# Performance work log

Hardware: AMD Instinct MI355X
Metric: run time of the kernel (lower is better)

The kernel has to match this reference:

```python
import math
import jax, jax.numpy as jnp
import numpy as np

B, D, CTX, HID, NSTEPS = 16384, 16, 256, 192, 10
IN_DIM = D + CTX + 1  # 273
DT = -0.1  # integrate t: 1 -> 0 in 10 fixed RK4 steps


def setup_inputs() -> dict:
    key = jax.random.key(0)
    ks = jax.random.split(key, 9)
    rn = lambda k, shape, sc=1.0: jax.random.normal(k, shape, dtype=jnp.float32) * sc
    return {
        "theta": rn(ks[0], (B, D)),
        "h": rn(ks[1], (B, CTX)),
        "eps": rn(ks[2], (NSTEPS, 4, B, D)),  # fresh Hutchinson noise per RK4 stage
        "W1": rn(ks[3], (IN_DIM, HID), 0.5 / np.sqrt(IN_DIM)),
        "b1": jnp.zeros((HID,), jnp.float32),
        "W2": rn(ks[4], (HID, HID), 0.5 / np.sqrt(HID)),
        "b2": jnp.zeros((HID,), jnp.float32),
        "W3": rn(ks[5], (HID, D), 0.5 / np.sqrt(HID)),
        "b3": jnp.zeros((D,), jnp.float32),
    }


def _mlp(x, W1, b1, W2, b2, W3, b3):
    # CNF_MLP depth=2: Linear->GELU->Linear->GELU->Linear (exact erf GELU, torch default)
    h1 = jax.nn.gelu(x @ W1 + b1, approximate=False)
    h2 = jax.nn.gelu(h1 @ W2 + b2, approximate=False)
    return h2 @ W3 + b3


def reference(theta, h, eps, W1, b1, W2, b2, W3, b3):
    """ConditionalCNF.log_prob: RK4 (torchdiffeq 3/8 variant) from t=1 to t=0
    with Hutchinson trace estimator via JVP (eps^T J eps)."""
    dt = jnp.float32(DT)

    def vf(t, y, e):
        def net(y_):
            tf = jnp.full((y_.shape[0], 1), t, y_.dtype)
            return _mlp(jnp.concatenate([y_, h, tf], axis=1), W1, b1, W2, b2, W3, b3)
        f, Je = jax.jvp(net, (y,), (e,))  # Je = J @ e
        trace = jnp.sum(e * Je, axis=1)   # eps^T J eps == (J^T eps) . eps
        return f, -trace

    def step(carry, xs):
        y, logp = carry
        t, e4 = xs  # e4: (4, B, D)
        f1, l1 = vf(t, y, e4[0])
        f2, l2 = vf(t + dt / 3, y + dt * f1 / 3, e4[1])
        f3, l3 = vf(t + 2 * dt / 3, y + dt * (f2 - f1 / 3), e4[2])
        f4, l4 = vf(t + dt, y + dt * (f1 - f2 + f3), e4[3])
        y2 = y + dt * (f1 + 3 * (f2 + f3) + f4) * 0.125
        lp2 = logp + dt * (l1 + 3 * (l2 + l3) + l4) * 0.125
        return (y2, lp2), None

    ts = jnp.float32(1.0) + dt * jnp.arange(NSTEPS, dtype=jnp.float32)
    logp0 = jnp.zeros((theta.shape[0],), theta.dtype)
    (z0, dlogp), _ = jax.lax.scan(step, (theta, logp0), (ts, eps))
    base = -0.5 * jnp.sum(z0 ** 2, axis=1) - 0.5 * D * math.log(2 * math.pi)
    return base - dlogp
```

## Files before the change

### kernel.cpp

```cpp
#include <hip/hip_runtime.h>
#include <math.h>


#define DTc (-0.1f)

typedef __attribute__((ext_vector_type(8))) short bf16x8;
typedef __attribute__((ext_vector_type(8))) unsigned short u16x8;
typedef __attribute__((ext_vector_type(4))) float f32x4;

#define MFMA16(a, b, c) __builtin_amdgcn_mfma_f32_16x16x32_bf16((a), (b), (c), 0, 0, 0)

__device__ __forceinline__ unsigned short f2bf(float x) {
    union { float f; unsigned int u; } c; c.f = x;
    unsigned int r = c.u + 0x7FFFu + ((c.u >> 16) & 1u);
    return (unsigned short)(r >> 16);
}

__device__ __forceinline__ unsigned int pk2bf(float lo, float hi) {
#if __has_builtin(__builtin_amdgcn_cvt_pk_bf16_f32)
    auto v = __builtin_amdgcn_cvt_pk_bf16_f32(lo, hi);
    return __builtin_bit_cast(unsigned int, v);
#else
    return (unsigned int)f2bf(lo) | ((unsigned int)f2bf(hi) << 16);
#endif
}

__device__ __forceinline__ void gelu_both(float x, float& gv, float& dv) {
    float z  = fabsf(x) * 0.70710678118654752f;
    float e  = __builtin_amdgcn_exp2f(x * x * -0.72134752044448170f);
    float t  = __builtin_amdgcn_rcpf(__builtin_fmaf(0.3275911f, z, 1.0f));
    float p  = t * (0.127414796f + t * (-0.142248368f + t * (0.710706871f +
               t * (-0.726576014f + t * 0.530702715f))));
    float ch = p * e;
    float cdf = (x >= 0.0f) ? (1.0f - ch) : ch;
    gv = x * cdf;
    dv = __builtin_fmaf(0.39894228040143268f * x, e, cdf);
}

__global__ void repack_kernel(const float* __restrict__ W1, const float* __restrict__ W2,
                              const float* __restrict__ W3,
                              unsigned short* __restrict__ w2f, unsigned short* __restrict__ w1yf,
                              unsigned short* __restrict__ w1cf, unsigned short* __restrict__ w3fg) {
    int t = blockIdx.x * 256 + threadIdx.x;
    u16x8 v;
    if (t < 4608) {
        int kb = t / 768, rem = t % 768, nt = rem / 64, lane = rem % 64;
        int n = nt * 16 + (lane & 15), k0 = kb * 32 + (lane >> 4) * 8;
        #pragma unroll
        for (int j = 0; j < 8; ++j) v[j] = f2bf(W2[(k0 + j) * 192 + n]);
        *(u16x8*)(w2f + t * 8) = v;
    } else if (t < 5376) {
        int i2 = t - 4608, nt = i2 / 64, lane = i2 % 64;
        int n = nt * 16 + (lane & 15), k0 = (lane >> 4) * 8;
        #pragma unroll
        for (int j = 0; j < 8; ++j) {
            int k = k0 + j;
            v[j] = (k < 16) ? f2bf(W1[k * 192 + n]) : (unsigned short)0;
        }
        *(u16x8*)(w1yf + i2 * 8) = v;
    } else if (t < 11520) {
        int i3 = t - 5376, kb = i3 / 768, rem = i3 % 768, nt = rem / 64, lane = rem % 64;
        int n = nt * 16 + (lane & 15), k0 = kb * 32 + (lane >> 4) * 8;
        #pragma unroll
        for (int j = 0; j < 8; ++j) v[j] = f2bf(W1[(16 + k0 + j) * 192 + n]);
        *(u16x8*)(w1cf + i3 * 8) = v;
    } else if (t < 11904) {
        int i4 = t - 11520, kb = i4 / 64, lane = i4 % 64;
        int n = lane & 15, k0 = kb * 32 + (lane >> 4) * 8;
        #pragma unroll
        for (int j = 0; j < 8; ++j) v[j] = f2bf(W3[(k0 + j) * 16 + n]);
        *(u16x8*)(w3fg + i4 * 8) = v;
    }
}

__global__ __launch_bounds__(256, 2) void cnf_mfma(
    const float* __restrict__ theta, const float* __restrict__ hctx,
    const float* __restrict__ eps,   const float* __restrict__ W1,
    const float* __restrict__ b1,    const float* __restrict__ b2,
    const float* __restrict__ b3,
    const unsigned short* __restrict__ w2f, const unsigned short* __restrict__ w1yf,
    const unsigned short* __restrict__ w1cf, const unsigned short* __restrict__ w3fg,
    float* __restrict__ out)
{
    __shared__ __align__(16) unsigned short Y[64 * 40];
    __shared__ __align__(16) unsigned short Xa0[64 * 200];
    __shared__ __align__(16) unsigned short Xa1[64 * 200];
    __shared__ __align__(16) float ebf[2][512];
    __shared__ float trx[32];

    const int tid  = threadIdx.x;
    const int wave = tid >> 6, lane = tid & 63;
    const int l15  = lane & 15, quad = lane >> 4;
    const int r0   = blockIdx.x * 32;
    const int ntg0 = wave * 3;

    for (int i = tid; i < 64 * 40; i += 256) Y[i] = 0;

    unsigned short* Hs = Xa0;
    for (int t4 = tid; t4 < 2048; t4 += 256) {
        int r = t4 >> 6, k = (t4 & 63) * 4;
        float4 v = *(const float4*)(hctx + (long)(r0 + r) * 256 + k);
        *(uint2*)(&Hs[r * 264 + k]) = make_uint2(pk2bf(v.x, v.y), pk2bf(v.z, v.w));
    }

    const int  ek = ((wave - 2) * 64 + lane) * 4;
    const int  er = ek >> 4, ed = ek & 15;
    const long epsBase = (long)r0 * 16 + ek;
    float4 epr;
    if (wave >= 2) epr = *(const float4*)(eps + epsBase);

    bf16x8 b1yfr[3], w3fr[6];
    #pragma unroll
    for (int nt = 0; nt < 3; ++nt)
        b1yfr[nt] = *reinterpret_cast<const bf16x8*>(w1yf + ((ntg0 + nt) * 64 + lane) * 8);
    #pragma unroll
    for (int kb = 0; kb < 6; ++kb)
        w3fr[kb] = *reinterpret_cast<const bf16x8*>(w3fg + (kb * 64 + lane) * 8);
    float w1tr[3], b2r[3], b1r[3];
    #pragma unroll
    for (int nt = 0; nt < 3; ++nt) {
        int n = (ntg0 + nt) * 16 + l15;
        w1tr[nt] = W1[272 * 192 + n];
        b2r[nt]  = b2[n];
        b1r[nt]  = b1[n];
    }
    const float b3r = b3[l15];

    float yreg[2][4];
    if (wave == 0) {
        #pragma unroll
        for (int mt = 0; mt < 2; ++mt)
            #pragma unroll
            for (int i = 0; i < 4; ++i)
                yreg[mt][i] = theta[(r0 + mt * 16 + quad * 4 + i) * 16 + l15];
    }

    __syncthreads();

    float cr[2][3][4];
    {
        f32x4 ca[2][3] = {};
        #pragma unroll
        for (int kb = 0; kb < 8; ++kb) {
            bf16x8 af[2];
            #pragma unroll
            for (int mt = 0; mt < 2; ++mt)
                af[mt] = *reinterpret_cast<const bf16x8*>(&Hs[(mt * 16 + l15) * 264 + kb * 32 + quad * 8]);
            #pragma unroll
            for (int nt = 0; nt < 3; ++nt) {
                bf16x8 bf = *reinterpret_cast<const bf16x8*>(w1cf + ((kb * 12 + ntg0 + nt) * 64 + lane) * 8);
                #pragma unroll
                for (int mt = 0; mt < 2; ++mt)
                    ca[mt][nt] = MFMA16(af[mt], bf, ca[mt][nt]);
            }
        }
        #pragma unroll
        for (int mt = 0; mt < 2; ++mt)
            #pragma unroll
            for (int nt = 0; nt < 3; ++nt)
                #pragma unroll
                for (int i = 0; i < 4; ++i)
                    cr[mt][nt][i] = ca[mt][nt][i] + b1r[nt];
    }

    if (wave == 0) {
        #pragma unroll
        for (int mt = 0; mt < 2; ++mt)
            #pragma unroll
            for (int i = 0; i < 4; ++i)
                Y[(mt * 16 + quad * 4 + i) * 40 + l15] = f2bf(yreg[mt][i]);
    }
    if (wave >= 2) {
        *(uint2*)(&Y[(32 + er) * 40 + ed]) = make_uint2(pk2bf(epr.x, epr.y), pk2bf(epr.z, epr.w));
        *(float4*)(&ebf[0][ek]) = epr;
        epr = *(const float4*)(eps + (long)1 * 262144 + epsBase);
    }

    float F1[2][4], F2[2][4], F3[2][4];
    float tracc[2][4] = {{0.f,0.f,0.f,0.f},{0.f,0.f,0.f,0.f}};

    for (int sg = 0; sg < 40; ++sg) {
        const int sub = sg & 3;
        const float ts = 1.0f + DTc * (float)(sg >> 2) + DTc * ((float)sub * (1.0f / 3.0f));

        __syncthreads();

        {
            bf16x8 af[4];
            #pragma unroll
            for (int mt = 0; mt < 4; ++mt)
                af[mt] = *reinterpret_cast<const bf16x8*>(&Y[(mt * 16 + l15) * 40 + quad * 8]);
            f32x4 acc[4][3] = {};
            #pragma unroll
            for (int nt = 0; nt < 3; ++nt)
                #pragma unroll
                for (int mt = 0; mt < 4; ++mt)
                    acc[mt][nt] = MFMA16(af[mt], b1yfr[nt], acc[mt][nt]);
            #pragma unroll
            for (int nt = 0; nt < 3; ++nt) {
                int n = (ntg0 + nt) * 16 + l15;
                #pragma unroll
                for (int mt = 0; mt < 2; ++mt) {
                    float gvv[4], dvv[4];
                    #pragma unroll
                    for (int i = 0; i < 4; ++i) {
                        float a = acc[mt][nt][i] + cr[mt][nt][i] + ts * w1tr[nt];
                        float gv, dv; gelu_both(a, gv, dv);
                        gvv[i] = gv; dvv[i] = dv * acc[mt + 2][nt][i];
                    }
                    unsigned int p0 = pk2bf(gvv[0], gvv[1]), p1 = pk2bf(gvv[2], gvv[3]);
                    unsigned int q0 = pk2bf(dvv[0], dvv[1]), q1 = pk2bf(dvv[2], dvv[3]);
                    int ba = (mt * 16 + quad * 4) * 200 + n;
                    Xa0[ba]          = (unsigned short)p0;
                    Xa0[ba + 200]    = (unsigned short)(p0 >> 16);
                    Xa0[ba + 400]    = (unsigned short)p1;
                    Xa0[ba + 600]    = (unsigned short)(p1 >> 16);
                    Xa0[ba + 6400]   = (unsigned short)q0;
                    Xa0[ba + 6600]   = (unsigned short)(q0 >> 16);
                    Xa0[ba + 6800]   = (unsigned short)q1;
                    Xa0[ba + 7000]   = (unsigned short)(q1 >> 16);
                }
            }
        }
        __syncthreads();

        {
            f32x4 acc2[4][3] = {};
            #pragma unroll
            for (int kb = 0; kb < 6; ++kb) {
                bf16x8 aA[4];
                #pragma unroll
                for (int mt = 0; mt < 4; ++mt)
                    aA[mt] = *reinterpret_cast<const bf16x8*>(&Xa0[(mt * 16 + l15) * 200 + kb * 32 + quad * 8]);
                #pragma unroll
                for (int nt = 0; nt < 3; ++nt) {
                    bf16x8 bf = *reinterpret_cast<const bf16x8*>(w2f + ((kb * 12 + ntg0 + nt) * 64 + lane) * 8);
                    #pragma unroll
                    for (int mt = 0; mt < 4; ++mt)
                        acc2[mt][nt] = MFMA16(aA[mt], bf, acc2[mt][nt]);
                }
            }
            #pragma unroll
            for (int nt = 0; nt < 3; ++nt) {
                int n = (ntg0 + nt) * 16 + l15;
                #pragma unroll
                for (int mt = 0; mt < 2; ++mt) {
                    float gvv[4], dvv[4];
                    #pragma unroll
                    for (int i = 0; i < 4; ++i) {
                        float a = acc2[mt][nt][i] + b2r[nt];
                        float gv, dv; gelu_both(a, gv, dv);
                        gvv[i] = gv; dvv[i] = dv * acc2[mt + 2][nt][i];
                    }
                    unsigned int p0 = pk2bf(gvv[0], gvv[1]), p1 = pk2bf(gvv[2], gvv[3]);
                    unsigned int q0 = pk2bf(dvv[0], dvv[1]), q1 = pk2bf(dvv[2], dvv[3]);
                    int ba = (mt * 16 + quad * 4) * 200 + n;
                    Xa1[ba]          = (unsigned short)p0;
                    Xa1[ba + 200]    = (unsigned short)(p0 >> 16);
                    Xa1[ba + 400]    = (unsigned short)p1;
                    Xa1[ba + 600]    = (unsigned short)(p1 >> 16);
                    Xa1[ba + 6400]   = (unsigned short)q0;
                    Xa1[ba + 6600]   = (unsigned short)(q0 >> 16);
                    Xa1[ba + 6800]   = (unsigned short)q1;
                    Xa1[ba + 7000]   = (unsigned short)(q1 >> 16);
                }
            }
        }
        __syncthreads();

        if (wave < 2) {
            f32x4 acc3[2] = {};
            #pragma unroll
            for (int kb = 0; kb < 6; ++kb)
                #pragma unroll
                for (int mt = 0; mt < 2; ++mt) {
                    bf16x8 af = *reinterpret_cast<const bf16x8*>(
                        &Xa1[(wave * 32 + mt * 16 + l15) * 200 + kb * 32 + quad * 8]);
                    acc3[mt] = MFMA16(af, w3fr[kb], acc3[mt]);
                }

            if (wave == 0) {
                float Fc[2][4];
                #pragma unroll
                for (int mt = 0; mt < 2; ++mt)
                    #pragma unroll
                    for (int i = 0; i < 4; ++i) Fc[mt][i] = acc3[mt][i] + b3r;
                if (sub == 0) {
                    #pragma unroll
                    for (int mt = 0; mt < 2; ++mt)
                        for (int i = 0; i < 4; ++i) F1[mt][i] = Fc[mt][i];
                } else if (sub == 1) {
                    #pragma unroll
                    for (int mt = 0; mt < 2; ++mt)
                        for (int i = 0; i < 4; ++i) F2[mt][i] = Fc[mt][i];
                } else if (sub == 2) {
                    #pragma unroll
                    for (int mt = 0; mt < 2; ++mt)
                        for (int i = 0; i < 4; ++i) F3[mt][i] = Fc[mt][i];
                } else {
                    #pragma unroll
                    for (int mt = 0; mt < 2; ++mt)
                        #pragma unroll
                        for (int i = 0; i < 4; ++i)
                            yreg[mt][i] += DTc * 0.125f *
                                (F1[mt][i] + 3.0f * (F2[mt][i] + F3[mt][i]) + Fc[mt][i]);
                }
                if (sg < 39) {
                    const int sub2 = (sg + 1) & 3;
                    #pragma unroll
                    for (int mt = 0; mt < 2; ++mt)
                        #pragma unroll
                        for (int i = 0; i < 4; ++i) {
                            float ys = yreg[mt][i];
                            if (sub2 == 1)      ys += DTc * (1.0f / 3.0f) * F1[mt][i];
                            else if (sub2 == 2) ys += DTc * (F2[mt][i] - (1.0f / 3.0f) * F1[mt][i]);
                            else if (sub2 == 3) ys += DTc * (F1[mt][i] - F2[mt][i] + F3[mt][i]);
                            Y[(mt * 16 + quad * 4 + i) * 40 + l15] = f2bf(ys);
                        }
                }
            } else {
                const float csub = (sub == 1 || sub == 2) ? 3.0f : 1.0f;
                #pragma unroll
                for (int mt = 0; mt < 2; ++mt)
                    #pragma unroll
                    for (int i = 0; i < 4; ++i) {
                        int r = mt * 16 + quad * 4 + i;
                        float p = ebf[sg & 1][r * 16 + l15] * acc3[mt][i];
                        p += __shfl_xor(p, 1);
                        p += __shfl_xor(p, 2);
                        p += __shfl_xor(p, 4);
                        p += __shfl_xor(p, 8);
                        tracc[mt][i] += csub * p;
                    }
            }
        } else {
            if (sg < 39) {
                *(uint2*)(&Y[(32 + er) * 40 + ed]) = make_uint2(pk2bf(epr.x, epr.y), pk2bf(epr.z, epr.w));
                *(float4*)(&ebf[(sg + 1) & 1][ek]) = epr;
                if (sg < 38)
                    epr = *(const float4*)(eps + (long)(sg + 2) * 262144 + epsBase);
            }
        }
    }

    if (wave == 1 && l15 == 0) {
        #pragma unroll
        for (int mt = 0; mt < 2; ++mt)
            #pragma unroll
            for (int i = 0; i < 4; ++i) trx[mt * 16 + quad * 4 + i] = tracc[mt][i];
    }
    __syncthreads();
    if (wave == 0) {
        #pragma unroll
        for (int mt = 0; mt < 2; ++mt)
            #pragma unroll
            for (int i = 0; i < 4; ++i) {
                float q = yreg[mt][i] * yreg[mt][i];
                q += __shfl_xor(q, 1);
                q += __shfl_xor(q, 2);
                q += __shfl_xor(q, 4);
                q += __shfl_xor(q, 8);
                if (l15 == 0)
                    out[r0 + mt * 16 + quad * 4 + i] =
                        -0.5f * q - 14.7030165313f + DTc * 0.125f * trx[mt * 16 + quad * 4 + i];
            }
    }
}

extern "C" void kernel_launch(void* const* d_in, const int* in_sizes, int n_in,
                              void* d_out, int out_size, void* d_ws, size_t ws_size,
                              hipStream_t stream) {
    const float* theta = (const float*)d_in[0];
    const float* hctx  = (const float*)d_in[1];
    const float* eps   = (const float*)d_in[2];
    const float* W1    = (const float*)d_in[3];
    const float* b1    = (const float*)d_in[4];
    const float* W2    = (const float*)d_in[5];
    const float* b2    = (const float*)d_in[6];
    const float* W3    = (const float*)d_in[7];
    const float* b3    = (const float*)d_in[8];
    float* outp = (float*)d_out;

    unsigned short* w2f  = (unsigned short*)d_ws;
    unsigned short* w1yf = w2f + 36864;
    unsigned short* w1cf = w1yf + 6144;
    unsigned short* w3fg = w1cf + 49152;

    hipLaunchKernelGGL(repack_kernel, dim3(47), dim3(256), 0, stream,
                       W1, W2, W3, w2f, w1yf, w1cf, w3fg);
    hipLaunchKernelGGL(cnf_mfma, dim3(512), dim3(256), 0, stream,
                       theta, hctx, eps, W1, b1, b2, b3, w2f, w1yf, w1cf, w3fg, outp);
}
```

Measured before the change: 400.1 us.

## Compute Hutchinson trace via W3ᵀε projection, drop layer-3 tangent GEMM

The trace eps^T J eps is now computed as a dot product of the layer-2 tangent with W3ᵀε, done by a small MFMA. This removes the second-layer tangent rows from the layer-3 GEMM and from shared memory, and makes Xa1 half as large. The time input is folded into the layer-1 MFMA as an extra K column, and eps is loaded straight into registers with prefetch instead of being staged through LDS by two dedicated waves. The erf polynomial is also cut to a lower-order approximation (3 terms), which trades GELU accuracy for fewer instructions.

```diff
diff --git a/kernel.cpp b/kernel.cpp
--- a/kernel.cpp
+++ b/kernel.cpp
@@ -28,9 +28,8 @@
 __device__ __forceinline__ void gelu_both(float x, float& gv, float& dv) {
     float z  = fabsf(x) * 0.70710678118654752f;
     float e  = __builtin_amdgcn_exp2f(x * x * -0.72134752044448170f);
-    float t  = __builtin_amdgcn_rcpf(__builtin_fmaf(0.3275911f, z, 1.0f));
-    float p  = t * (0.127414796f + t * (-0.142248368f + t * (0.710706871f +
-               t * (-0.726576014f + t * 0.530702715f))));
+    float t  = __builtin_amdgcn_rcpf(__builtin_fmaf(0.47047f, z, 1.0f));
+    float p  = t * (0.1740121f + t * (-0.0479399f + t * 0.3739278f));
     float ch = p * e;
     float cdf = (x >= 0.0f) ? (1.0f - ch) : ch;
     gv = x * cdf;
@@ -40,7 +39,8 @@
 __global__ void repack_kernel(const float* __restrict__ W1, const float* __restrict__ W2,
                               const float* __restrict__ W3,
                               unsigned short* __restrict__ w2f, unsigned short* __restrict__ w1yf,
-                              unsigned short* __restrict__ w1cf, unsigned short* __restrict__ w3fg) {
+                              unsigned short* __restrict__ w1cf, unsigned short* __restrict__ w3fg,
+                              unsigned short* __restrict__ w3tf) {
     int t = blockIdx.x * 256 + threadIdx.x;
     u16x8 v;
     if (t < 4608) {
@@ -55,7 +55,8 @@
         #pragma unroll
         for (int j = 0; j < 8; ++j) {
             int k = k0 + j;
-            v[j] = (k < 16) ? f2bf(W1[k * 192 + n]) : (unsigned short)0;
+            v[j] = (k < 16) ? f2bf(W1[k * 192 + n])
+                 : (k == 16) ? f2bf(W1[272 * 192 + n]) : (unsigned short)0;
         }
         *(u16x8*)(w1yf + i2 * 8) = v;
     } else if (t < 11520) {
@@ -70,31 +71,40 @@
         #pragma unroll
         for (int j = 0; j < 8; ++j) v[j] = f2bf(W3[(k0 + j) * 16 + n]);
         *(u16x8*)(w3fg + i4 * 8) = v;
+    } else if (t < 12672) {
+        int i5 = t - 11904, nt = i5 / 64, lane = i5 % 64;
+        int h = nt * 16 + (lane & 15), quad = lane >> 4;
+        #pragma unroll
+        for (int j = 0; j < 8; ++j) {
+            int d = quad * 8 + j;
+            v[j] = (d < 16) ? f2bf(W3[h * 16 + d]) : (unsigned short)0;
+        }
+        *(u16x8*)(w3tf + i5 * 8) = v;
     }
 }
 
 __global__ __launch_bounds__(256, 2) void cnf_mfma(
     const float* __restrict__ theta, const float* __restrict__ hctx,
-    const float* __restrict__ eps,   const float* __restrict__ W1,
-    const float* __restrict__ b1,    const float* __restrict__ b2,
-    const float* __restrict__ b3,
+    const float* __restrict__ eps,   const float* __restrict__ b1,
+    const float* __restrict__ b2,    const float* __restrict__ b3,
     const unsigned short* __restrict__ w2f, const unsigned short* __restrict__ w1yf,
     const unsigned short* __restrict__ w1cf, const unsigned short* __restrict__ w3fg,
+    const unsigned short* __restrict__ w3tf,
     float* __restrict__ out)
 {
-    __shared__ __align__(16) unsigned short Y[64 * 40];
+    __shared__ __align__(16) unsigned short Ys[32 * 24];
     __shared__ __align__(16) unsigned short Xa0[64 * 200];
-    __shared__ __align__(16) unsigned short Xa1[64 * 200];
-    __shared__ __align__(16) float ebf[2][512];
-    __shared__ float trx[32];
+    __shared__ __align__(16) unsigned short Xa1[32 * 200];
+    __shared__ float trrow[32];
 
     const int tid  = threadIdx.x;
     const int wave = tid >> 6, lane = tid & 63;
     const int l15  = lane & 15, quad = lane >> 4;
     const int r0   = blockIdx.x * 32;
     const int ntg0 = wave * 3;
-
-    for (int i = tid; i < 64 * 40; i += 256) Y[i] = 0;
+    const int mt3  = wave - 2;
+
+    if (tid < 32) trrow[tid] = 0.0f;
 
     unsigned short* Hs = Xa0;
     for (int t4 = tid; t4 < 2048; t4 += 256) {
@@ -103,36 +113,42 @@
         *(uint2*)(&Hs[r * 264 + k]) = make_uint2(pk2bf(v.x, v.y), pk2bf(v.z, v.w));
     }
 
-    const int  ek = ((wave - 2) * 64 + lane) * 4;
-    const int  er = ek >> 4, ed = ek & 15;
-    const long epsBase = (long)r0 * 16 + ek;
-    float4 epr;
-    if (wave >= 2) epr = *(const float4*)(eps + epsBase);
-
     bf16x8 b1yfr[3], w3fr[6];
     #pragma unroll
     for (int nt = 0; nt < 3; ++nt)
         b1yfr[nt] = *reinterpret_cast<const bf16x8*>(w1yf + ((ntg0 + nt) * 64 + lane) * 8);
-    #pragma unroll
-    for (int kb = 0; kb < 6; ++kb)
-        w3fr[kb] = *reinterpret_cast<const bf16x8*>(w3fg + (kb * 64 + lane) * 8);
-    float w1tr[3], b2r[3], b1r[3];
+    if (wave >= 2) {
+        #pragma unroll
+        for (int kb = 0; kb < 6; ++kb)
+            w3fr[kb] = *reinterpret_cast<const bf16x8*>(w3fg + (kb * 64 + lane) * 8);
+    }
+    float b2r[3], b1r[3];
     #pragma unroll
     for (int nt = 0; nt < 3; ++nt) {
         int n = (ntg0 + nt) * 16 + l15;
-        w1tr[nt] = W1[272 * 192 + n];
-        b2r[nt]  = b2[n];
-        b1r[nt]  = b1[n];
+        b2r[nt] = b2[n];
+        b1r[nt] = b1[n];
     }
     const float b3r = b3[l15];
 
-    float yreg[2][4];
-    if (wave == 0) {
-        #pragma unroll
-        for (int mt = 0; mt < 2; ++mt)
-            #pragma unroll
-            for (int i = 0; i < 4; ++i)
-                yreg[mt][i] = theta[(r0 + mt * 16 + quad * 4 + i) * 16 + l15];
+    float yreg[4];
+    if (wave >= 2) {
+        #pragma unroll
+        for (int i = 0; i < 4; ++i)
+            yreg[i] = theta[(r0 + mt3 * 16 + quad * 4 + i) * 16 + l15];
+    }
+
+    bf16x8 e0 = {}, e1 = {};
+    if (quad < 2) {
+        const float* ep = eps + ((long)r0 + l15) * 16 + quad * 8;
+        float4 a0 = *(const float4*)ep,          a1 = *(const float4*)(ep + 4);
+        float4 b0 = *(const float4*)(ep + 256),  b4 = *(const float4*)(ep + 260);
+        union { unsigned int u[4]; bf16x8 v; } c0, c1;
+        c0.u[0] = pk2bf(a0.x, a0.y); c0.u[1] = pk2bf(a0.z, a0.w);
+        c0.u[2] = pk2bf(a1.x, a1.y); c0.u[3] = pk2bf(a1.z, a1.w);
+        c1.u[0] = pk2bf(b0.x, b0.y); c1.u[1] = pk2bf(b0.z, b0.w);
+        c1.u[2] = pk2bf(b4.x, b4.y); c1.u[3] = pk2bf(b4.z, b4.w);
+        e0 = c0.v; e1 = c1.v;
     }
 
     __syncthreads();
@@ -163,207 +179,201 @@
                     cr[mt][nt][i] = ca[mt][nt][i] + b1r[nt];
     }
 
-    if (wave == 0) {
-        #pragma unroll
-        for (int mt = 0; mt < 2; ++mt)
-            #pragma unroll
-            for (int i = 0; i < 4; ++i)
-                Y[(mt * 16 + quad * 4 + i) * 40 + l15] = f2bf(yreg[mt][i]);
-    }
     if (wave >= 2) {
-        *(uint2*)(&Y[(32 + er) * 40 + ed]) = make_uint2(pk2bf(epr.x, epr.y), pk2bf(epr.z, epr.w));
-        *(float4*)(&ebf[0][ek]) = epr;
-        epr = *(const float4*)(eps + (long)1 * 262144 + epsBase);
-    }
-
-    float F1[2][4], F2[2][4], F3[2][4];
+        #pragma unroll
+        for (int i = 0; i < 4; ++i)
+            Ys[(mt3 * 16 + quad * 4 + i) * 24 + l15] = f2bf(yreg[i]);
+    }
+
+    float F1[4], F2[4], F3[4];
     float tracc[2][4] = {{0.f,0.f,0.f,0.f},{0.f,0.f,0.f,0.f}};
 
     for (int sg = 0; sg < 40; ++sg) {
         const int sub = sg & 3;
         const float ts = 1.0f + DTc * (float)(sg >> 2) + DTc * ((float)sub * (1.0f / 3.0f));
+        const short tsb = (short)f2bf(ts);
 
         __syncthreads();
 
+        bf16x8 aY0 = {}, aY1 = {};
+        if (quad < 2) {
+            aY0 = *reinterpret_cast<const bf16x8*>(&Ys[l15 * 24 + quad * 8]);
+            aY1 = *reinterpret_cast<const bf16x8*>(&Ys[(16 + l15) * 24 + quad * 8]);
+        } else if (quad == 2) {
+            aY0[0] = tsb; aY1[0] = tsb;
+        }
+
+        f32x4 uacc[2][3] = {};
+        f32x4 acc[4][3]  = {};
+        #pragma unroll
+        for (int nt = 0; nt < 3; ++nt) {
+            bf16x8 w3t = *reinterpret_cast<const bf16x8*>(w3tf + ((ntg0 + nt) * 64 + lane) * 8);
+            uacc[0][nt] = MFMA16(e0, w3t, uacc[0][nt]);
+            uacc[1][nt] = MFMA16(e1, w3t, uacc[1][nt]);
+            acc[0][nt] = MFMA16(aY0, b1yfr[nt], acc[0][nt]);
+            acc[1][nt] = MFMA16(aY1, b1yfr[nt], acc[1][nt]);
+            acc[2][nt] = MFMA16(e0,  b1yfr[nt], acc[2][nt]);
+            acc[3][nt] = MFMA16(e1,  b1yfr[nt], acc[3][nt]);
+        }
+
+        float4 pa0, pa1, pb0, pb1;
+        if (sg < 39 && quad < 2) {
+            const float* ep = eps + ((long)(sg + 1) * 16384 + r0 + l15) * 16 + quad * 8;
+            pa0 = *(const float4*)ep;         pa1 = *(const float4*)(ep + 4);
+            pb0 = *(const float4*)(ep + 256); pb1 = *(const float4*)(ep + 260);
+        }
+
+        #pragma unroll
+        for (int nt = 0; nt < 3; ++nt) {
+            int n = (ntg0 + nt) * 16 + l15;
+            #pragma unroll
+            for (int mt = 0; mt < 2; ++mt) {
+                float gvv[4], dvv[4];
+                #pragma unroll
+                for (int i = 0; i < 4; ++i) {
+                    float a = acc[mt][nt][i] + cr[mt][nt][i];
+                    float gv, dv; gelu_both(a, gv, dv);
+                    gvv[i] = gv; dvv[i] = dv * acc[mt + 2][nt][i];
+                }
+                unsigned int p0 = pk2bf(gvv[0], gvv[1]), p1 = pk2bf(gvv[2], gvv[3]);
+                unsigned int q0 = pk2bf(dvv[0], dvv[1]), q1 = pk2bf(dvv[2], dvv[3]);
+                int ba = (mt * 16 + quad * 4) * 200 + n;
+                Xa0[ba]          = (unsigned short)p0;
+                Xa0[ba + 200]    = (unsigned short)(p0 >> 16);
+                Xa0[ba + 400]    = (unsigned short)p1;
+                Xa0[ba + 600]    = (unsigned short)(p1 >> 16);
+                Xa0[ba + 6400]   = (unsigned short)q0;
+                Xa0[ba + 6600]   = (unsigned short)(q0 >> 16);
+                Xa0[ba + 6800]   = (unsigned short)q1;
+                Xa0[ba + 7000]   = (unsigned short)(q1 >> 16);
+            }
+        }
+        __syncthreads();
+
+        f32x4 acc2[4][3] = {};
+        #pragma unroll
+        for (int kb = 0; kb < 6; ++kb) {
+            bf16x8 aA[4];
+            #pragma unroll
+            for (int mt = 0; mt < 4; ++mt)
+                aA[mt] = *reinterpret_cast<const bf16x8*>(&Xa0[(mt * 16 + l15) * 200 + kb * 32 + quad * 8]);
+            #pragma unroll
+            for (int nt = 0; nt < 3; ++nt) {
+                bf16x8 bf = *reinterpret_cast<const bf16x8*>(w2f + ((kb * 12 + ntg0 + nt) * 64 + lane) * 8);
+                #pragma unroll
+                for (int mt = 0; mt < 4; ++mt)
+                    acc2[mt][nt] = MFMA16(aA[mt], bf, acc2[mt][nt]);
+            }
+        }
+
         {
-            bf16x8 af[4];
-            #pragma unroll
-            for (int mt = 0; mt < 4; ++mt)
-                af[mt] = *reinterpret_cast<const bf16x8*>(&Y[(mt * 16 + l15) * 40 + quad * 8]);
-            f32x4 acc[4][3] = {};
-            #pragma unroll
-            for (int nt = 0; nt < 3; ++nt)
-                #pragma unroll
-                for (int mt = 0; mt < 4; ++mt)
-                    acc[mt][nt] = MFMA16(af[mt], b1yfr[nt], acc[mt][nt]);
+            float tsum[2][4] = {{0.f,0.f,0.f,0.f},{0.f,0.f,0.f,0.f}};
             #pragma unroll
             for (int nt = 0; nt < 3; ++nt) {
                 int n = (ntg0 + nt) * 16 + l15;
                 #pragma unroll
                 for (int mt = 0; mt < 2; ++mt) {
-                    float gvv[4], dvv[4];
-                    #pragma unroll
-                    for (int i = 0; i < 4; ++i) {
-                        float a = acc[mt][nt][i] + cr[mt][nt][i] + ts * w1tr[nt];
-                        float gv, dv; gelu_both(a, gv, dv);
-                        gvv[i] = gv; dvv[i] = dv * acc[mt + 2][nt][i];
-                    }
-                    unsigned int p0 = pk2bf(gvv[0], gvv[1]), p1 = pk2bf(gvv[2], gvv[3]);
-                    unsigned int q0 = pk2bf(dvv[0], dvv[1]), q1 = pk2bf(dvv[2], dvv[3]);
-                    int ba = (mt * 16 + quad * 4) * 200 + n;
-                    Xa0[ba]          = (unsigned short)p0;
-                    Xa0[ba + 200]    = (unsigned short)(p0 >> 16);
-                    Xa0[ba + 400]    = (unsigned short)p1;
-                    Xa0[ba + 600]    = (unsigned short)(p1 >> 16);
-                    Xa0[ba + 6400]   = (unsigned short)q0;
-                    Xa0[ba + 6600]   = (unsigned short)(q0 >> 16);
-                    Xa0[ba + 6800]   = (unsigned short)q1;
-                    Xa0[ba + 7000]   = (unsigned short)(q1 >> 16);
-                }
-            }
-        }
-        __syncthreads();
-
-        {
-            f32x4 acc2[4][3] = {};
-            #pragma unroll
-            for (int kb = 0; kb < 6; ++kb) {
-                bf16x8 aA[4];
-                #pragma unroll
-                for (int mt = 0; mt < 4; ++mt)
-                    aA[mt] = *reinterpret_cast<const bf16x8*>(&Xa0[(mt * 16 + l15) * 200 + kb * 32 + quad * 8]);
-                #pragma unroll
-                for (int nt = 0; nt < 3; ++nt) {
-                    bf16x8 bf = *reinterpret_cast<const bf16x8*>(w2f + ((kb * 12 + ntg0 + nt) * 64 + lane) * 8);
-                    #pragma unroll
-                    for (int mt = 0; mt < 4; ++mt)
-                        acc2[mt][nt] = MFMA16(aA[mt], bf, acc2[mt][nt]);
-                }
-            }
-            #pragma unroll
-            for (int nt = 0; nt < 3; ++nt) {
-                int n = (ntg0 + nt) * 16 + l15;
-                #pragma unroll
-                for (int mt = 0; mt < 2; ++mt) {
-                    float gvv[4], dvv[4];
+                    float gvv[4];
                     #pragma unroll
                     for (int i = 0; i < 4; ++i) {
                         float a = acc2[mt][nt][i] + b2r[nt];
                         float gv, dv; gelu_both(a, gv, dv);
-                        gvv[i] = gv; dvv[i] = dv * acc2[mt + 2][nt][i];
+                        gvv[i] = gv;
+                        float dh2 = dv * acc2[mt + 2][nt][i];
+                        tsum[mt][i] = __builtin_fmaf(dh2, uacc[mt][nt][i], tsum[mt][i]);
                     }
                     unsigned int p0 = pk2bf(gvv[0], gvv[1]), p1 = pk2bf(gvv[2], gvv[3]);
-                    unsigned int q0 = pk2bf(dvv[0], dvv[1]), q1 = pk2bf(dvv[2], dvv[3]);
                     int ba = (mt * 16 + quad * 4) * 200 + n;
-                    Xa1[ba]          = (unsigned short)p0;
-                    Xa1[ba + 200]    = (unsigned short)(p0 >> 16);
-                    Xa1[ba + 400]    = (unsigned short)p1;
-                    Xa1[ba + 600]    = (unsigned short)(p1 >> 16);
-                    Xa1[ba + 6400]   = (unsigned short)q0;
-                    Xa1[ba + 6600]   = (unsigned short)(q0 >> 16);
-                    Xa1[ba + 6800]   = (unsigned short)q1;
-                    Xa1[ba + 7000]   = (unsigned short)(q1 >> 16);
+                    Xa1[ba]       = (unsigned short)p0;
+                    Xa1[ba + 200] = (unsigned short)(p0 >> 16);
+                    Xa1[ba + 400] = (unsigned short)p1;
+                    Xa1[ba + 600] = (unsigned short)(p1 >> 16);
                 }
             }
+            const float csub = (sub == 1 || sub == 2) ? 3.0f : 1.0f;
+            #pragma unroll
+            for (int mt = 0; mt < 2; ++mt)
+                #pragma unroll
+                for (int i = 0; i < 4; ++i)
+                    tracc[mt][i] = __builtin_fmaf(csub, tsum[mt][i], tracc[mt][i]);
         }
         __syncthreads();
 
-        if (wave < 2) {
-            f32x4 acc3[2] = {};
+        if (wave >= 2) {
+            f32x4 acc3 = {};
+            const unsigned short* src = &Xa1[(mt3 * 16 + l15) * 200];
             #pragma unroll
             for (int kb = 0; kb < 6; ++kb)
-                #pragma unroll
-                for (int mt = 0; mt < 2; ++mt) {
-                    bf16x8 af = *reinterpret_cast<const bf16x8*>(
-                        &Xa1[(wave * 32 + mt * 16 + l15) * 200 + kb * 32 + quad * 8]);
-                    acc3[mt] = MFMA16(af, w3fr[kb], acc3[mt]);
+                acc3 = MFMA16(*reinterpret_cast<const bf16x8*>(src + kb * 32 + quad * 8), w3fr[kb], acc3);
+            float Fc[4];
+            #pragma unroll
+            for (int i = 0; i < 4; ++i) Fc[i] = acc3[i] + b3r;
+            if (sub == 0) {
+                #pragma unroll
+                for (int i = 0; i < 4; ++i) F1[i] = Fc[i];
+            } else if (sub == 1) {
+                #pragma unroll
+                for (int i = 0; i < 4; ++i) F2[i] = Fc[i];
+            } else if (sub == 2) {
+                #pragma unroll
+                for (int i = 0; i < 4; ++i) F3[i] = Fc[i];
+            } else {
+                #pragma unroll
+                for (int i = 0; i < 4; ++i)
+                    yreg[i] += DTc * 0.125f * (F1[i] + 3.0f * (F2[i] + F3[i]) + Fc[i]);
+            }
+            if (sg < 39) {
+                const int sub2 = (sg + 1) & 3;
+                #pragma unroll
+                for (int i = 0; i < 4; ++i) {
+                    float ys = yreg[i];
+                    if (sub2 == 1)      ys += DTc * (1.0f / 3.0f) * F1[i];
+                    else if (sub2 == 2) ys += DTc * (F2[i] - (1.0f / 3.0f) * F1[i]);
+                    else if (sub2 == 3) ys += DTc * (F1[i] - F2[i] + F3[i]);
+                    Ys[(mt3 * 16 + quad * 4 + i) * 24 + l15] = f2bf(ys);
                 }
-
-            if (wave == 0) {
-                float Fc[2][4];
-                #pragma unroll
-                for (int mt = 0; mt < 2; ++mt)
-                    #pragma unroll
-                    for (int i = 0; i < 4; ++i) Fc[mt][i] = acc3[mt][i] + b3r;
-                if (sub == 0) {
-                    #pragma unroll
-                    for (int mt = 0; mt < 2; ++mt)
-                        for (int i = 0; i < 4; ++i) F1[mt][i] = Fc[mt][i];
-                } else if (sub == 1) {
-                    #pragma unroll
-                    for (int mt = 0; mt < 2; ++mt)
-                        for (int i = 0; i < 4; ++i) F2[mt][i] = Fc[mt][i];
-                } else if (sub == 2) {
-                    #pragma unroll
-                    for (int mt = 0; mt < 2; ++mt)
-                        for (int i = 0; i < 4; ++i) F3[mt][i] = Fc[mt][i];
-                } else {
-                    #pragma unroll
-                    for (int mt = 0; mt < 2; ++mt)
-                        #pragma unroll
-                        for (int i = 0; i < 4; ++i)
-                            yreg[mt][i] += DTc * 0.125f *
-                                (F1[mt][i] + 3.0f * (F2[mt][i] + F3[mt][i]) + Fc[mt][i]);
-                }
-                if (sg < 39) {
-                    const int sub2 = (sg + 1) & 3;
-                    #pragma unroll
-                    for (int mt = 0; mt < 2; ++mt)
-                        #pragma unroll
-                        for (int i = 0; i < 4; ++i) {
-                            float ys = yreg[mt][i];
-                            if (sub2 == 1)      ys += DTc * (1.0f / 3.0f) * F1[mt][i];
-                            else if (sub2 == 2) ys += DTc * (F2[mt][i] - (1.0f / 3.0f) * F1[mt][i]);
-                            else if (sub2 == 3) ys += DTc * (F1[mt][i] - F2[mt][i] + F3[mt][i]);
-                            Y[(mt * 16 + quad * 4 + i) * 40 + l15] = f2bf(ys);
-                        }
-                }
-            } else {
-                const float csub = (sub == 1 || sub == 2) ? 3.0f : 1.0f;
-                #pragma unroll
-                for (int mt = 0; mt < 2; ++mt)
-                    #pragma unroll
-                    for (int i = 0; i < 4; ++i) {
-                        int r = mt * 16 + quad * 4 + i;
-                        float p = ebf[sg & 1][r * 16 + l15] * acc3[mt][i];
-                        p += __shfl_xor(p, 1);
-                        p += __shfl_xor(p, 2);
-                        p += __shfl_xor(p, 4);
-                        p += __shfl_xor(p, 8);
-                        tracc[mt][i] += csub * p;
-                    }
-            }
-        } else {
-            if (sg < 39) {
-                *(uint2*)(&Y[(32 + er) * 40 + ed]) = make_uint2(pk2bf(epr.x, epr.y), pk2bf(epr.z, epr.w));
-                *(float4*)(&ebf[(sg + 1) & 1][ek]) = epr;
-                if (sg < 38)
-                    epr = *(const float4*)(eps + (long)(sg + 2) * 262144 + epsBase);
-            }
-        }
-    }
-
-    if (wave == 1 && l15 == 0) {
-        #pragma unroll
-        for (int mt = 0; mt < 2; ++mt)
-            #pragma unroll
-            for (int i = 0; i < 4; ++i) trx[mt * 16 + quad * 4 + i] = tracc[mt][i];
-    }
+            }
+        }
+
+        if (sg < 39) {
+            e0 = bf16x8{}; e1 = bf16x8{};
+            if (quad < 2) {
+                union { unsigned int u[4]; bf16x8 v; } c0, c1;
+                c0.u[0] = pk2bf(pa0.x, pa0.y); c0.u[1] = pk2bf(pa0.z, pa0.w);
+                c0.u[2] = pk2bf(pa1.x, pa1.y); c0.u[3] = pk2bf(pa1.z, pa1.w);
+                c1.u[0] = pk2bf(pb0.x, pb0.y); c1.u[1] = pk2bf(pb0.z, pb0.w);
+                c1.u[2] = pk2bf(pb1.x, pb1.y); c1.u[3] = pk2bf(pb1.z, pb1.w);
+                e0 = c0.v; e1 = c1.v;
+            }
+        }
+    }
+
+    #pragma unroll
+    for (int mt = 0; mt < 2; ++mt)
+        #pragma unroll
+        for (int i = 0; i < 4; ++i) {
+            float v = tracc[mt][i];
+            v += __shfl_xor(v, 1);
+            v += __shfl_xor(v, 2);
+            v += __shfl_xor(v, 4);
+            v += __shfl_xor(v, 8);
+            if (l15 == 0) atomicAdd(&trrow[mt * 16 + quad * 4 + i], v);
+        }
     __syncthreads();
-    if (wave == 0) {
-        #pragma unroll
-        for (int mt = 0; mt < 2; ++mt)
-            #pragma unroll
-            for (int i = 0; i < 4; ++i) {
-                float q = yreg[mt][i] * yreg[mt][i];
-                q += __shfl_xor(q, 1);
-                q += __shfl_xor(q, 2);
-                q += __shfl_xor(q, 4);
-                q += __shfl_xor(q, 8);
-                if (l15 == 0)
-                    out[r0 + mt * 16 + quad * 4 + i] =
-                        -0.5f * q - 14.7030165313f + DTc * 0.125f * trx[mt * 16 + quad * 4 + i];
-            }
+
+    if (wave >= 2) {
+        #pragma unroll
+        for (int i = 0; i < 4; ++i) {
+            float q = yreg[i] * yreg[i];
+            q += __shfl_xor(q, 1);
+            q += __shfl_xor(q, 2);
+            q += __shfl_xor(q, 4);
+            q += __shfl_xor(q, 8);
+            if (l15 == 0) {
+                int r = mt3 * 16 + quad * 4 + i;
+                out[r0 + r] = -0.5f * q - 14.7030165313f + DTc * 0.125f * trrow[r];
+            }
+        }
     }
 }
 
@@ -385,9 +395,10 @@
     unsigned short* w1yf = w2f + 36864;
     unsigned short* w1cf = w1yf + 6144;
     unsigned short* w3fg = w1cf + 49152;
-
-    hipLaunchKernelGGL(repack_kernel, dim3(47), dim3(256), 0, stream,
-                       W1, W2, W3, w2f, w1yf, w1cf, w3fg);
+    unsigned short* w3tf = w3fg + 3072;
+
+    hipLaunchKernelGGL(repack_kernel, dim3(50), dim3(256), 0, stream,
+                       W1, W2, W3, w2f, w1yf, w1cf, w3fg, w3tf);
     hipLaunchKernelGGL(cnf_mfma, dim3(512), dim3(256), 0, stream,
-                       theta, hctx, eps, W1, b1, b2, b3, w2f, w1yf, w1cf, w3fg, outp);
-}
+                       theta, hctx, eps, b1, b2, b3, w2f, w1yf, w1cf, w3fg, w3tf, outp);
+}
```

New measurement: 829.2 us. 2.07x slower.
